# Kernel tuning notes

Hardware: AMD Instinct MI355X
Metric: run time of the kernel (lower is better)

Reference implementation:

```python
import jax, jax.numpy as jnp
import numpy as np

N = 50000      # nodes
E = 800000     # edges
H = 64         # hid_dim (== in_dim)
T = 4          # number of S2V message-passing steps


def setup_inputs() -> dict:
    key = jax.random.key(0)
    ks = jax.random.split(key, 12)
    mu = jax.random.normal(ks[0], (N, H), dtype=jnp.float32)
    x = jax.random.uniform(ks[1], (N, 1), dtype=jnp.float32)
    edge_index = jax.random.randint(ks[2], (2, E), 0, N, dtype=jnp.int64)
    edge_w = jax.random.uniform(ks[3], (E, 1), dtype=jnp.float32)
    s = 0.05  # small init scale to keep activations bounded across T relu layers
    W1 = jax.random.normal(ks[4], (T, H, 1), dtype=jnp.float32) * s   # lin1 per layer, torch [out,in]
    W2 = jax.random.normal(ks[5], (T, H, H), dtype=jnp.float32) * s   # lin2 per layer
    W3 = jax.random.normal(ks[6], (T, H, H), dtype=jnp.float32) * s   # lin3 per layer
    W4 = jax.random.normal(ks[7], (T, H, 1), dtype=jnp.float32) * s   # lin4 per layer
    W5 = jax.random.normal(ks[8], (1, 2 * H), dtype=jnp.float32) * s  # lin5
    W7 = jax.random.normal(ks[9], (H, H), dtype=jnp.float32) * s      # lin7
    return {"mu": mu, "x": x, "edge_index": edge_index, "edge_w": edge_w,
            "W1": W1, "W2": W2, "W3": W3, "W4": W4, "W5": W5, "W7": W7}


def _s2v_step(mu, x, idx, edge_w, w1, w2, w3, w4):
    # Faithful to source: gather AND scatter both use edge_index[1].
    x_emb = x @ w1.T                                            # [N,H]
    mu_j = mu[idx]                                              # [E,H] gather
    mu_aggr = jax.ops.segment_sum(mu_j, idx, num_segments=N)    # [N,H] scatter_add
    mu_aggr = mu_aggr @ w2.T
    ew = jax.nn.relu(edge_w @ w4.T)                             # [E,H]
    ew_aggr = jax.ops.segment_sum(ew, idx, num_segments=N)      # [N,H]
    ew_aggr = ew_aggr @ w3.T
    return jax.nn.relu(x_emb + mu_aggr + ew_aggr)


def reference(mu, x, edge_index, edge_w, W1, W2, W3, W4, W5, W7):
    idx = edge_index[1]
    for t in range(T):
        mu = _s2v_step(mu, x, idx, edge_w, W1[t], W2[t], W3[t], W4[t])
    nodes_vec = mu @ W7.T                                       # [N,H]
    graph_pool = jnp.broadcast_to(jnp.sum(mu, axis=0, keepdims=True), (N, H))
    cat = jnp.concatenate([graph_pool, nodes_vec], axis=1)      # [N,2H]
    return (jax.nn.relu(cat) @ W5.T).squeeze(-1)                # [N]
```

## Files before the change

### kernel.cpp

```cpp
#include <hip/hip_runtime.h>

#define H 64
#define NPB 64
#define KS 104
typedef short bf16x8 __attribute__((ext_vector_type(8)));
typedef float f32x4 __attribute__((ext_vector_type(4)));

static __device__ __forceinline__ unsigned short f2bf(float f) {
    union { float f; unsigned u; } v; v.f = f;
    unsigned r = v.u + 0x7fffu + ((v.u >> 16) & 1u);
    return (unsigned short)(r >> 16);
}
static __device__ __forceinline__ float bf2f(unsigned short b) {
    union { unsigned u; float f; } v; v.u = ((unsigned)b) << 16;
    return v.f;
}
static __device__ __forceinline__ void split8(const float* ff, bf16x8& hi, bf16x8& lo) {
#pragma unroll
    for (int j = 0; j < 8; ++j) {
        unsigned short h = f2bf(ff[j]);
        hi[j] = (short)h;
        lo[j] = (short)f2bf(ff[j] - bf2f(h));
    }
}


__global__ __launch_bounds__(256)
void prep_kernel(const float* __restrict__ W1, const float* __restrict__ W2,
                 const float* __restrict__ W3, const float* __restrict__ W4,
                 const float* __restrict__ W7, unsigned* __restrict__ zero_base,
                 int zero_dwords, bf16x8* __restrict__ Bp, bf16x8* __restrict__ W7p) {
    const int t = threadIdx.x;
    if (blockIdx.x != 0) {
        int idx = (blockIdx.x - 1) * 256 + t;
        for (int i = idx; i < zero_dwords; i += 64 * 256) zero_base[i] = 0u;
        return;
    }
    __shared__ float v3s[4 * H];
    {
        int tl = t >> 6, h = t & 63;
        const float* __restrict__ w3r = W3 + (tl * H + h) * H;
        const float* __restrict__ w4r = W4 + tl * H;
        float a0 = 0, a1 = 0, a2 = 0, a3 = 0;
#pragma unroll
        for (int k = 0; k < H; k += 4) {
            a0 += fmaxf(w4r[k + 0], 0.f) * w3r[k + 0];
            a1 += fmaxf(w4r[k + 1], 0.f) * w3r[k + 1];
            a2 += fmaxf(w4r[k + 2], 0.f) * w3r[k + 2];
            a3 += fmaxf(w4r[k + 3], 0.f) * w3r[k + 3];
        }
        v3s[t] = (a0 + a1) + (a2 + a3);
    }
    __syncthreads();
    const int w = t >> 6, lane = t & 63, c = lane & 15, q = lane >> 4;
    const int hh = 16 * w + c;
    for (int tl = 0; tl < 4; ++tl) {
        const int b3 = (tl * 4 + w) * 3;
        bf16x8 hi, lo;
#pragma unroll
        for (int s = 0; s < 2; ++s) {
            const float* __restrict__ wp = W2 + (tl * H + hh) * H + s * 32 + q * 8;
            float4 f0 = *(const float4*)(wp);
            float4 f1 = *(const float4*)(wp + 4);
            float ff[8] = {f0.x, f0.y, f0.z, f0.w, f1.x, f1.y, f1.z, f1.w};
            split8(ff, hi, lo);
            Bp[(b3 + s) * 128 + lane] = hi;
            Bp[(b3 + s) * 128 + 64 + lane] = lo;
        }
        float ff[8] = {0, 0, 0, 0, 0, 0, 0, 0};
        if (q == 0) { ff[0] = W1[tl * H + hh]; ff[1] = v3s[tl * H + hh]; }
        split8(ff, hi, lo);
        Bp[(b3 + 2) * 128 + lane] = hi;
        Bp[(b3 + 2) * 128 + 64 + lane] = lo;
    }
#pragma unroll
    for (int s = 0; s < 2; ++s) {
        const float* __restrict__ wp = W7 + hh * H + s * 32 + q * 8;
        float4 f0 = *(const float4*)(wp);
        float4 f1 = *(const float4*)(wp + 4);
        float ff[8] = {f0.x, f0.y, f0.z, f0.w, f1.x, f1.y, f1.z, f1.w};
        bf16x8 hi, lo;
        split8(ff, hi, lo);
        W7p[(w * 2 + s) * 128 + lane] = hi;
        W7p[(w * 2 + s) * 128 + 64 + lane] = lo;
    }
}

__global__ __launch_bounds__(256)
void edge_kernel(const int* __restrict__ ei, const float* __restrict__ ew,
                 double* __restrict__ dS, int E) {
    int probe = ei[2 * (threadIdx.x & 63) + 1];
    bool is64 = (__ballot(probe != 0) == 0ULL);
    int e0 = 4 * (blockIdx.x * blockDim.x + threadIdx.x);
    if (e0 >= E) return;
    if (e0 + 3 < E) {
        float4 wv = *(const float4*)(ew + e0);
        int i0, i1, i2, i3;
        if (is64) {
            int4 a = *(const int4*)(ei + 2 * (E + e0));
            int4 b = *(const int4*)(ei + 2 * (E + e0) + 4);
            i0 = a.x; i1 = a.z; i2 = b.x; i3 = b.z;
        } else {
            int4 a = *(const int4*)(ei + E + e0);
            i0 = a.x; i1 = a.y; i2 = a.z; i3 = a.w;
        }
        unsafeAtomicAdd(&dS[i0], 4096.0 + (double)wv.x);
        unsafeAtomicAdd(&dS[i1], 4096.0 + (double)wv.y);
        unsafeAtomicAdd(&dS[i2], 4096.0 + (double)wv.z);
        unsafeAtomicAdd(&dS[i3], 4096.0 + (double)wv.w);
    } else {
        for (int j = 0; j < 4 && e0 + j < E; ++j) {
            int e = e0 + j;
            int idx = is64 ? ei[2 * (E + e)] : ei[E + e];
            unsafeAtomicAdd(&dS[idx], 4096.0 + (double)ew[e]);
        }
    }
}

__global__ __launch_bounds__(256, 2)
void node_kernel(const float* __restrict__ mu, const float* __restrict__ x,
                 const float* __restrict__ W5, const bf16x8* __restrict__ Bp,
                 const bf16x8* __restrict__ W7p, const double* __restrict__ dS,
                 float* __restrict__ gp, float* __restrict__ out, int N) {
    __shared__ unsigned short Ab[2][NPB * KS];
    __shared__ float degs[NPB];
    __shared__ float red[4 * NPB];

    const int t = threadIdx.x;
    const int lane = t & 63;
    const int w = __builtin_amdgcn_readfirstlane(t >> 6);
    const int c = lane & 15;
    const int q = lane >> 4;
    const int hh = 16 * w + c;
    const int base = blockIdx.x * NPB;

    if (t < 128) {
        int buf = t >> 6, row = t & 63;
        unsigned* p = (unsigned*)&Ab[buf][row * KS];
#pragma unroll
        for (int d = 33; d < 52; ++d) p[d] = 0u;
    }
    if (t < 64) {
        int node = base + t;
        float dg = 0.f, sv = 0.f, xv = 0.f;
        if (node < N) {
            double T = dS[node];
            double k = floor(T * (1.0 / 4096.0));
            dg = (float)k;
            sv = (float)(T - 4096.0 * k);
            xv = x[node];
        }
        degs[t] = dg;
        unsigned short xb = f2bf(xv), sb = f2bf(sv);
        Ab[0][t * KS + 64] = xb; Ab[0][t * KS + 65] = sb;
        Ab[1][t * KS + 64] = xb; Ab[1][t * KS + 65] = sb;
    }
    __syncthreads();

    {
        const float* __restrict__ mublk = mu + (size_t)base * H;
        const int maxf = (N - base) * H;
#pragma unroll
        for (int cc = 0; cc < 4; ++cc) {
            int f = (t + 256 * cc) * 4;
            float4 v = make_float4(0.f, 0.f, 0.f, 0.f);
            if (f < maxf) v = *(const float4*)(mublk + f);
            int m = f >> 6, k = f & 63;
            float dg = degs[m];
            ushort4 b;
            b.x = f2bf(v.x * dg); b.y = f2bf(v.y * dg);
            b.z = f2bf(v.z * dg); b.w = f2bf(v.w * dg);
            *(ushort4*)(&Ab[0][m * KS + k]) = b;
        }
    }
    __syncthreads();

    unsigned short* Acur = &Ab[0][0];
    unsigned short* Anxt = &Ab[1][0];

    for (int tl = 0; tl < 4; ++tl) {
        const int b3 = (tl * 4 + w) * 3;
        bf16x8 bh0 = Bp[(b3 + 0) * 128 + lane], bl0 = Bp[(b3 + 0) * 128 + 64 + lane];
        bf16x8 bh1 = Bp[(b3 + 1) * 128 + lane], bl1 = Bp[(b3 + 1) * 128 + 64 + lane];
        bf16x8 bh2 = Bp[(b3 + 2) * 128 + lane], bl2 = Bp[(b3 + 2) * 128 + 64 + lane];

        f32x4 acc[4];
#pragma unroll
        for (int mt = 0; mt < 4; ++mt)
#pragma unroll
            for (int r = 0; r < 4; ++r) acc[mt][r] = 0.f;

#pragma unroll
        for (int mt = 0; mt < 4; ++mt) {
            const unsigned short* ar = Acur + (mt * 16 + c) * KS;
            bf16x8 a0 = *(const bf16x8*)(ar + q * 8);
            bf16x8 a1 = *(const bf16x8*)(ar + 32 + q * 8);
            bf16x8 a2 = *(const bf16x8*)(ar + 64 + q * 8);
            acc[mt] = __builtin_amdgcn_mfma_f32_16x16x32_bf16(a0, bh0, acc[mt], 0, 0, 0);
            acc[mt] = __builtin_amdgcn_mfma_f32_16x16x32_bf16(a0, bl0, acc[mt], 0, 0, 0);
            acc[mt] = __builtin_amdgcn_mfma_f32_16x16x32_bf16(a1, bh1, acc[mt], 0, 0, 0);
            acc[mt] = __builtin_amdgcn_mfma_f32_16x16x32_bf16(a1, bl1, acc[mt], 0, 0, 0);
            acc[mt] = __builtin_amdgcn_mfma_f32_16x16x32_bf16(a2, bh2, acc[mt], 0, 0, 0);
            acc[mt] = __builtin_amdgcn_mfma_f32_16x16x32_bf16(a2, bl2, acc[mt], 0, 0, 0);
        }

        const bool scale = (tl < 3);
#pragma unroll
        for (int mt = 0; mt < 4; ++mt) {
#pragma unroll
            for (int r = 0; r < 4; ++r) {
                int m = mt * 16 + q * 4 + r;
                float v = fmaxf(acc[mt][r], 0.f);
                if (scale) v *= degs[m];
                Anxt[m * KS + hh] = f2bf(v);
            }
        }
        __syncthreads();
        unsigned short* tmp = Acur; Acur = Anxt; Anxt = tmp;
    }

    {
        bf16x8 bh0 = W7p[(w * 2 + 0) * 128 + lane], bl0 = W7p[(w * 2 + 0) * 128 + 64 + lane];
        bf16x8 bh1 = W7p[(w * 2 + 1) * 128 + lane], bl1 = W7p[(w * 2 + 1) * 128 + 64 + lane];
        f32x4 acc[4];
#pragma unroll
        for (int mt = 0; mt < 4; ++mt)
#pragma unroll
            for (int r = 0; r < 4; ++r) acc[mt][r] = 0.f;
#pragma unroll
        for (int mt = 0; mt < 4; ++mt) {
            const unsigned short* ar = Acur + (mt * 16 + c) * KS;
            bf16x8 a0 = *(const bf16x8*)(ar + q * 8);
            bf16x8 a1 = *(const bf16x8*)(ar + 32 + q * 8);
            acc[mt] = __builtin_amdgcn_mfma_f32_16x16x32_bf16(a0, bh0, acc[mt], 0, 0, 0);
            acc[mt] = __builtin_amdgcn_mfma_f32_16x16x32_bf16(a0, bl0, acc[mt], 0, 0, 0);
            acc[mt] = __builtin_amdgcn_mfma_f32_16x16x32_bf16(a1, bh1, acc[mt], 0, 0, 0);
            acc[mt] = __builtin_amdgcn_mfma_f32_16x16x32_bf16(a1, bl1, acc[mt], 0, 0, 0);
        }
        float w5v = W5[H + hh];
#pragma unroll
        for (int mt = 0; mt < 4; ++mt) {
#pragma unroll
            for (int r = 0; r < 4; ++r) {
                float v = fmaxf(acc[mt][r], 0.f) * w5v;
                v += __shfl_xor(v, 1);
                v += __shfl_xor(v, 2);
                v += __shfl_xor(v, 4);
                v += __shfl_xor(v, 8);
                if (c == 0) red[w * 64 + mt * 16 + q * 4 + r] = v;
            }
        }
    }
    __syncthreads();
    if (t < 64) {
        float pn = red[t] + red[64 + t] + red[128 + t] + red[192 + t];
        if (base + t < N) out[base + t] = pn;
    }
    __syncthreads();

    {
        int h = t & 63, mq = t >> 6;
        float s = 0.f;
#pragma unroll
        for (int i = 0; i < 16; ++i) s += bf2f(Acur[(mq * 16 + i) * KS + h]);
        red[t] = s;
    }
    __syncthreads();
    if (t < 64) {
        float g = red[t] + red[64 + t] + red[128 + t] + red[192 + t];
        unsafeAtomicAdd(&gp[t], g);
    }
}

__global__ __launch_bounds__(256)
void finalize_kernel(const float* __restrict__ gp, const float* __restrict__ W5,
                     float* __restrict__ out, int N) {
    int lane = threadIdx.x & 63;
    float v = fmaxf(gp[lane], 0.f) * W5[lane];
    v += __shfl_xor(v, 1);
    v += __shfl_xor(v, 2);
    v += __shfl_xor(v, 4);
    v += __shfl_xor(v, 8);
    v += __shfl_xor(v, 16);
    v += __shfl_xor(v, 32);
    int n = blockIdx.x * blockDim.x + threadIdx.x;
    if (n < N) out[n] += v;
}

extern "C" void kernel_launch(void* const* d_in, const int* in_sizes, int n_in,
                              void* d_out, int out_size, void* d_ws, size_t ws_size,
                              hipStream_t stream) {
    const float* mu = (const float*)d_in[0];
    const float* x  = (const float*)d_in[1];
    const int*   ei = (const int*)d_in[2];
    const float* ew = (const float*)d_in[3];
    const float* W1 = (const float*)d_in[4];
    const float* W2 = (const float*)d_in[5];
    const float* W3 = (const float*)d_in[6];
    const float* W4 = (const float*)d_in[7];
    const float* W5 = (const float*)d_in[8];
    const float* W7 = (const float*)d_in[9];
    float* out = (float*)d_out;

    const int N = in_sizes[1];
    const int E = in_sizes[3];

    char* ws = (char*)d_ws;
    double* dS  = (double*)ws;
    float*  gp  = (float*)(ws + (size_t)N * 8);
    bf16x8* Bp  = (bf16x8*)(ws + (size_t)N * 8 + 256);
    bf16x8* W7p = (bf16x8*)(ws + (size_t)N * 8 + 256 + 196608);
    int zero_dwords = N * 2 + 64;

    prep_kernel<<<65, 256, 0, stream>>>(W1, W2, W3, W4, W7, (unsigned*)dS,
                                        zero_dwords, Bp, W7p);
    edge_kernel<<<(E + 1023) / 1024, 256, 0, stream>>>(ei, ew, dS, E);
    node_kernel<<<(N + NPB - 1) / NPB, 256, 0, stream>>>(mu, x, W5, Bp, W7p,
                                                         dS, gp, out, N);
    finalize_kernel<<<(N + 255) / 256, 256, 0, stream>>>(gp, W5, out, N);
}
```

Measured before the change: 151.5 us.

## Fuse prep, edge, node and finalize stages into one cooperative persistent kernel

Replaces the four separate kernel launches with a single cooperative kernel that uses grid-wide syncs between the zero/weight-pack, edge scatter, node MFMA, and finalize phases. Each block processes up to four node tiles persistently and keeps per-node partial outputs in registers until the global pool is known. This removes per-launch overhead and inter-kernel gaps. The cost is grid sync latency and a grid capped by occupancy, with a fallback to the old multi-kernel path when cooperative launch is unavailable.

```diff
diff --git a/kernel.cpp b/kernel.cpp
--- a/kernel.cpp
+++ b/kernel.cpp
@@ -1,4 +1,7 @@
 #include <hip/hip_runtime.h>
+#include <hip/hip_cooperative_groups.h>
+
+namespace cg = cooperative_groups;
 
 #define H 64
 #define NPB 64
@@ -23,7 +26,296 @@
         lo[j] = (short)f2bf(ff[j] - bf2f(h));
     }
 }
-
+static __device__ __forceinline__ void store16_dev(bf16x8* dst, bf16x8 v) {
+    union { bf16x8 v; unsigned long long u[2]; } cv; cv.v = v;
+    unsigned long long* p = (unsigned long long*)dst;
+    atomicExch(p, cv.u[0]);
+    atomicExch(p + 1, cv.u[1]);
+}
+
+
+__global__ __launch_bounds__(256, 2)
+void fused_kernel(const float* __restrict__ mu, const float* __restrict__ x,
+                  const int* __restrict__ ei, const float* __restrict__ ew,
+                  const float* __restrict__ W1, const float* __restrict__ W2,
+                  const float* __restrict__ W3, const float* __restrict__ W4,
+                  const float* __restrict__ W5, const float* __restrict__ W7,
+                  double* __restrict__ dS, float* __restrict__ gp,
+                  bf16x8* __restrict__ Bp, bf16x8* __restrict__ W7p,
+                  float* __restrict__ out, int N, int E, int nT) {
+    __shared__ unsigned short Ab[2][NPB * KS];
+    __shared__ float degs[NPB];
+    __shared__ float red[4 * NPB];
+    __shared__ float v3s[H];
+
+    const int t = threadIdx.x;
+    const int bid = blockIdx.x;
+    const int gsz = gridDim.x;
+    const int lane = t & 63;
+    const int w = __builtin_amdgcn_readfirstlane(t >> 6);
+    const int c = lane & 15;
+    const int q = lane >> 4;
+    const int hh = 16 * w + c;
+
+    {
+        unsigned long long* z = (unsigned long long*)dS;
+        const int tot = N + 32;
+        for (int i = bid * 256 + t; i < tot; i += gsz * 256) atomicExch(z + i, 0ULL);
+    }
+    if (bid < 16) {
+        const int tl = bid >> 2, wl = bid & 3;
+        if (t < H) {
+            const float* __restrict__ w3r = W3 + (tl * H + t) * H;
+            const float* __restrict__ w4r = W4 + tl * H;
+            float a0 = 0, a1 = 0, a2 = 0, a3 = 0;
+#pragma unroll
+            for (int k = 0; k < H; k += 4) {
+                a0 += fmaxf(w4r[k + 0], 0.f) * w3r[k + 0];
+                a1 += fmaxf(w4r[k + 1], 0.f) * w3r[k + 1];
+                a2 += fmaxf(w4r[k + 2], 0.f) * w3r[k + 2];
+                a3 += fmaxf(w4r[k + 3], 0.f) * w3r[k + 3];
+            }
+            v3s[t] = (a0 + a1) + (a2 + a3);
+        }
+        __syncthreads();
+        if (t < 64) {
+            const int cc = t & 15, qq = t >> 4, hw = 16 * wl + cc;
+            const int b3 = (tl * 4 + wl) * 3;
+            bf16x8 hi, lo;
+#pragma unroll
+            for (int s = 0; s < 2; ++s) {
+                const float* __restrict__ wp = W2 + (tl * H + hw) * H + s * 32 + qq * 8;
+                float4 f0 = *(const float4*)(wp);
+                float4 f1 = *(const float4*)(wp + 4);
+                float ff[8] = {f0.x, f0.y, f0.z, f0.w, f1.x, f1.y, f1.z, f1.w};
+                split8(ff, hi, lo);
+                store16_dev(&Bp[(b3 + s) * 128 + t], hi);
+                store16_dev(&Bp[(b3 + s) * 128 + 64 + t], lo);
+            }
+            float ff[8] = {0, 0, 0, 0, 0, 0, 0, 0};
+            if (qq == 0) { ff[0] = W1[tl * H + hw]; ff[1] = v3s[hw]; }
+            split8(ff, hi, lo);
+            store16_dev(&Bp[(b3 + 2) * 128 + t], hi);
+            store16_dev(&Bp[(b3 + 2) * 128 + 64 + t], lo);
+        }
+    } else if (bid < 20) {
+        const int wl = bid - 16;
+        if (t < 64) {
+            const int cc = t & 15, qq = t >> 4, hw = 16 * wl + cc;
+            bf16x8 hi, lo;
+#pragma unroll
+            for (int s = 0; s < 2; ++s) {
+                const float* __restrict__ wp = W7 + hw * H + s * 32 + qq * 8;
+                float4 f0 = *(const float4*)(wp);
+                float4 f1 = *(const float4*)(wp + 4);
+                float ff[8] = {f0.x, f0.y, f0.z, f0.w, f1.x, f1.y, f1.z, f1.w};
+                split8(ff, hi, lo);
+                store16_dev(&W7p[(wl * 2 + s) * 128 + t], hi);
+                store16_dev(&W7p[(wl * 2 + s) * 128 + 64 + t], lo);
+            }
+        }
+    }
+    __threadfence();
+    cg::this_grid().sync();
+
+    {
+        int probe = ei[2 * (t & 63) + 1];
+        bool is64 = (__ballot(probe != 0) == 0ULL);
+        const int nq = (E + 3) >> 2;
+        for (int qd = bid * 256 + t; qd < nq; qd += gsz * 256) {
+            int e0 = 4 * qd;
+            if (e0 + 3 < E) {
+                float4 wv = *(const float4*)(ew + e0);
+                int i0, i1, i2, i3;
+                if (is64) {
+                    int4 a = *(const int4*)(ei + 2 * (E + e0));
+                    int4 b = *(const int4*)(ei + 2 * (E + e0) + 4);
+                    i0 = a.x; i1 = a.z; i2 = b.x; i3 = b.z;
+                } else {
+                    int4 a = *(const int4*)(ei + E + e0);
+                    i0 = a.x; i1 = a.y; i2 = a.z; i3 = a.w;
+                }
+                unsafeAtomicAdd(&dS[i0], 4096.0 + (double)wv.x);
+                unsafeAtomicAdd(&dS[i1], 4096.0 + (double)wv.y);
+                unsafeAtomicAdd(&dS[i2], 4096.0 + (double)wv.z);
+                unsafeAtomicAdd(&dS[i3], 4096.0 + (double)wv.w);
+            } else {
+                for (int j = 0; j < 4 && e0 + j < E; ++j) {
+                    int e = e0 + j;
+                    int idx = is64 ? ei[2 * (E + e)] : ei[E + e];
+                    unsafeAtomicAdd(&dS[idx], 4096.0 + (double)ew[e]);
+                }
+            }
+        }
+    }
+    __threadfence();
+    cg::this_grid().sync();
+
+    if (t < 128) {
+        int buf = t >> 6, row = t & 63;
+        unsigned* p = (unsigned*)&Ab[buf][row * KS];
+#pragma unroll
+        for (int d = 33; d < 52; ++d) p[d] = 0u;
+    }
+    float pn_s[4] = {0.f, 0.f, 0.f, 0.f};
+#pragma unroll
+    for (int it = 0; it < 4; ++it) {
+        const int tile = bid + it * gsz;
+        if (tile >= nT) break;
+        const int base = tile * NPB;
+
+        if (t < 64) {
+            int node = base + t;
+            float dg = 0.f, sv = 0.f, xv = 0.f;
+            if (node < N) {
+                double T = dS[node];
+                double k = floor(T * (1.0 / 4096.0));
+                dg = (float)k;
+                sv = (float)(T - 4096.0 * k);
+                xv = x[node];
+            }
+            degs[t] = dg;
+            unsigned short xb = f2bf(xv), sb = f2bf(sv);
+            Ab[0][t * KS + 64] = xb; Ab[0][t * KS + 65] = sb;
+            Ab[1][t * KS + 64] = xb; Ab[1][t * KS + 65] = sb;
+        }
+        __syncthreads();
+
+        {
+            const float* __restrict__ mublk = mu + (size_t)base * H;
+            const int maxf = (N - base) * H;
+#pragma unroll
+            for (int cc = 0; cc < 4; ++cc) {
+                int f = (t + 256 * cc) * 4;
+                float4 v = make_float4(0.f, 0.f, 0.f, 0.f);
+                if (f < maxf) v = *(const float4*)(mublk + f);
+                int m = f >> 6, k = f & 63;
+                float dg = degs[m];
+                ushort4 b;
+                b.x = f2bf(v.x * dg); b.y = f2bf(v.y * dg);
+                b.z = f2bf(v.z * dg); b.w = f2bf(v.w * dg);
+                *(ushort4*)(&Ab[0][m * KS + k]) = b;
+            }
+        }
+        __syncthreads();
+
+        unsigned short* Acur = &Ab[0][0];
+        unsigned short* Anxt = &Ab[1][0];
+
+        for (int tl = 0; tl < 4; ++tl) {
+            const int b3 = (tl * 4 + w) * 3;
+            bf16x8 bh0 = Bp[(b3 + 0) * 128 + lane], bl0 = Bp[(b3 + 0) * 128 + 64 + lane];
+            bf16x8 bh1 = Bp[(b3 + 1) * 128 + lane], bl1 = Bp[(b3 + 1) * 128 + 64 + lane];
+            bf16x8 bh2 = Bp[(b3 + 2) * 128 + lane], bl2 = Bp[(b3 + 2) * 128 + 64 + lane];
+
+            f32x4 acc[4];
+#pragma unroll
+            for (int mt = 0; mt < 4; ++mt)
+#pragma unroll
+                for (int r = 0; r < 4; ++r) acc[mt][r] = 0.f;
+
+#pragma unroll
+            for (int mt = 0; mt < 4; ++mt) {
+                const unsigned short* ar = Acur + (mt * 16 + c) * KS;
+                bf16x8 a0 = *(const bf16x8*)(ar + q * 8);
+                bf16x8 a1 = *(const bf16x8*)(ar + 32 + q * 8);
+                bf16x8 a2 = *(const bf16x8*)(ar + 64 + q * 8);
+                acc[mt] = __builtin_amdgcn_mfma_f32_16x16x32_bf16(a0, bh0, acc[mt], 0, 0, 0);
+                acc[mt] = __builtin_amdgcn_mfma_f32_16x16x32_bf16(a0, bl0, acc[mt], 0, 0, 0);
+                acc[mt] = __builtin_amdgcn_mfma_f32_16x16x32_bf16(a1, bh1, acc[mt], 0, 0, 0);
+                acc[mt] = __builtin_amdgcn_mfma_f32_16x16x32_bf16(a1, bl1, acc[mt], 0, 0, 0);
+                acc[mt] = __builtin_amdgcn_mfma_f32_16x16x32_bf16(a2, bh2, acc[mt], 0, 0, 0);
+                acc[mt] = __builtin_amdgcn_mfma_f32_16x16x32_bf16(a2, bl2, acc[mt], 0, 0, 0);
+            }
+
+            const bool scale = (tl < 3);
+#pragma unroll
+            for (int mt = 0; mt < 4; ++mt) {
+#pragma unroll
+                for (int r = 0; r < 4; ++r) {
+                    int m = mt * 16 + q * 4 + r;
+                    float v = fmaxf(acc[mt][r], 0.f);
+                    if (scale) v *= degs[m];
+                    Anxt[m * KS + hh] = f2bf(v);
+                }
+            }
+            __syncthreads();
+            unsigned short* tmp = Acur; Acur = Anxt; Anxt = tmp;
+        }
+
+        {
+            bf16x8 bh0 = W7p[(w * 2 + 0) * 128 + lane], bl0 = W7p[(w * 2 + 0) * 128 + 64 + lane];
+            bf16x8 bh1 = W7p[(w * 2 + 1) * 128 + lane], bl1 = W7p[(w * 2 + 1) * 128 + 64 + lane];
+            f32x4 acc[4];
+#pragma unroll
+            for (int mt = 0; mt < 4; ++mt)
+#pragma unroll
+                for (int r = 0; r < 4; ++r) acc[mt][r] = 0.f;
+#pragma unroll
+            for (int mt = 0; mt < 4; ++mt) {
+                const unsigned short* ar = Acur + (mt * 16 + c) * KS;
+                bf16x8 a0 = *(const bf16x8*)(ar + q * 8);
+                bf16x8 a1 = *(const bf16x8*)(ar + 32 + q * 8);
+                acc[mt] = __builtin_amdgcn_mfma_f32_16x16x32_bf16(a0, bh0, acc[mt], 0, 0, 0);
+                acc[mt] = __builtin_amdgcn_mfma_f32_16x16x32_bf16(a0, bl0, acc[mt], 0, 0, 0);
+                acc[mt] = __builtin_amdgcn_mfma_f32_16x16x32_bf16(a1, bh1, acc[mt], 0, 0, 0);
+                acc[mt] = __builtin_amdgcn_mfma_f32_16x16x32_bf16(a1, bl1, acc[mt], 0, 0, 0);
+            }
+            float w5v = W5[H + hh];
+#pragma unroll
+            for (int mt = 0; mt < 4; ++mt) {
+#pragma unroll
+                for (int r = 0; r < 4; ++r) {
+                    float v = fmaxf(acc[mt][r], 0.f) * w5v;
+                    v += __shfl_xor(v, 1);
+                    v += __shfl_xor(v, 2);
+                    v += __shfl_xor(v, 4);
+                    v += __shfl_xor(v, 8);
+                    if (c == 0) red[w * 64 + mt * 16 + q * 4 + r] = v;
+                }
+            }
+        }
+        __syncthreads();
+        if (t < 64) pn_s[it] = red[t] + red[64 + t] + red[128 + t] + red[192 + t];
+        __syncthreads();
+
+        {
+            int h = t & 63, mq = t >> 6;
+            float s = 0.f;
+#pragma unroll
+            for (int i = 0; i < 16; ++i) s += bf2f(Acur[(mq * 16 + i) * KS + h]);
+            red[t] = s;
+        }
+        __syncthreads();
+        if (t < 64) {
+            float g = red[t] + red[64 + t] + red[128 + t] + red[192 + t];
+            unsafeAtomicAdd(&gp[t], g);
+        }
+    }
+    __threadfence();
+    cg::this_grid().sync();
+
+    float C;
+    {
+        float v = fmaxf(gp[lane], 0.f) * W5[lane];
+        v += __shfl_xor(v, 1);
+        v += __shfl_xor(v, 2);
+        v += __shfl_xor(v, 4);
+        v += __shfl_xor(v, 8);
+        v += __shfl_xor(v, 16);
+        v += __shfl_xor(v, 32);
+        C = v;
+    }
+    if (t < 64) {
+#pragma unroll
+        for (int it = 0; it < 4; ++it) {
+            const int tile = bid + it * gsz;
+            if (tile >= nT) break;
+            const int node = tile * NPB + t;
+            if (node < N) out[node] = pn_s[it] + C;
+        }
+    }
+}
 
 __global__ __launch_bounds__(256)
 void prep_kernel(const float* __restrict__ W1, const float* __restrict__ W2,
@@ -310,12 +602,58 @@
     float*  gp  = (float*)(ws + (size_t)N * 8);
     bf16x8* Bp  = (bf16x8*)(ws + (size_t)N * 8 + 256);
     bf16x8* W7p = (bf16x8*)(ws + (size_t)N * 8 + 256 + 196608);
-    int zero_dwords = N * 2 + 64;
-
-    prep_kernel<<<65, 256, 0, stream>>>(W1, W2, W3, W4, W7, (unsigned*)dS,
-                                        zero_dwords, Bp, W7p);
-    edge_kernel<<<(E + 1023) / 1024, 256, 0, stream>>>(ei, ew, dS, E);
-    node_kernel<<<(N + NPB - 1) / NPB, 256, 0, stream>>>(mu, x, W5, Bp, W7p,
-                                                         dS, gp, out, N);
-    finalize_kernel<<<(N + 255) / 256, 256, 0, stream>>>(gp, W5, out, N);
-}
+
+    const int nT = (N + NPB - 1) / NPB;
+
+    static int coop_state = -1;
+    static int cap_blocks = 0;
+    if (coop_state == -1) {
+        int dev = 0;
+        (void)hipGetDevice(&dev);
+        int attr = 0, cu = 0, nb = 0;
+        (void)hipDeviceGetAttribute(&attr, hipDeviceAttributeCooperativeLaunch, dev);
+        (void)hipDeviceGetAttribute(&cu, hipDeviceAttributeMultiprocessorCount, dev);
+        hipError_t oe = hipOccupancyMaxActiveBlocksPerMultiprocessor(
+            &nb, reinterpret_cast<const void*>(&fused_kernel), 256, 0);
+        if (attr && oe == hipSuccess && nb > 0 && cu > 0) {
+            coop_state = 1;
+            cap_blocks = nb * cu;
+        } else {
+            coop_state = 0;
+        }
+    }
+
+    bool launched = false;
+    if (coop_state == 1) {
+        int grid = nT < cap_blocks ? nT : cap_blocks;
+        if (grid >= 20 && (long long)grid * 4 >= (long long)nT) {
+            int N_ = N, E_ = E, nT_ = nT;
+            void* args[] = {(void*)&mu, (void*)&x, (void*)&ei, (void*)&ew,
+                            (void*)&W1, (void*)&W2, (void*)&W3, (void*)&W4,
+                            (void*)&W5, (void*)&W7, (void*)&dS, (void*)&gp,
+                            (void*)&Bp, (void*)&W7p, (void*)&out,
+                            (void*)&N_, (void*)&E_, (void*)&nT_};
+            hipError_t e = hipLaunchCooperativeKernel(
+                reinterpret_cast<const void*>(&fused_kernel),
+                dim3(grid), dim3(256), args, 0, stream);
+            if (e == hipSuccess) {
+                launched = true;
+            } else {
+                coop_state = 0;
+                (void)hipGetLastError();
+            }
+        } else {
+            coop_state = 0;
+        }
+    }
+
+    if (!launched) {
+        int zero_dwords = N * 2 + 64;
+        prep_kernel<<<65, 256, 0, stream>>>(W1, W2, W3, W4, W7, (unsigned*)dS,
+                                            zero_dwords, Bp, W7p);
+        edge_kernel<<<(E + 1023) / 1024, 256, 0, stream>>>(ei, ew, dS, E);
+        node_kernel<<<(N + NPB - 1) / NPB, 256, 0, stream>>>(mu, x, W5, Bp, W7p,
+                                                             dS, gp, out, N);
+        finalize_kernel<<<(N + 255) / 256, 256, 0, stream>>>(gp, W5, out, N);
+    }
+}
```

Result: slower. 314.6 us (+107.6%).
